# Optimization experiments

Hardware: AMD Instinct MI355X
Metric: run time of the kernel (lower is better)

The kernel has to match this reference:

```python
import jax, jax.numpy as jnp
import numpy as np

N = 100000
E = 1600000
IN_CH = 128
HID = 16
HEADS = 4
OUT_CH = 2
EDGE_DIM = 3
NEG_SLOPE = 0.2


def gat_layer(x, src, dst, e_feat, W, att_src, att_dst, We, att_edge, bias, H, C, concat):
    # x: [N, Fin] -> projected [N, H, C]
    xs = (x @ W).reshape(-1, H, C)
    a_src = jnp.sum(xs * att_src, axis=-1)          # [N, H]
    a_dst = jnp.sum(xs * att_dst, axis=-1)          # [N, H]
    ee = (e_feat @ We).reshape(-1, H, C)            # [E, H, C]
    a_edge = jnp.sum(ee * att_edge, axis=-1)        # [E, H]
    alpha = a_src[src] + a_dst[dst] + a_edge        # [E, H]
    alpha = jax.nn.leaky_relu(alpha, NEG_SLOPE)
    # segment softmax over incoming edges of each dst node
    seg_max = jax.ops.segment_max(alpha, dst, num_segments=N)
    alpha = jnp.exp(alpha - seg_max[dst])
    seg_sum = jax.ops.segment_sum(alpha, dst, num_segments=N)
    alpha = alpha / (seg_sum[dst] + 1e-16)
    # weighted message aggregation
    msg = xs[src] * alpha[:, :, None]               # [E, H, C]
    out = jax.ops.segment_sum(msg, dst, num_segments=N)  # [N, H, C]
    out = out.reshape(-1, H * C) if concat else out.mean(axis=1)
    return out + bias


def setup_inputs() -> dict:
    key = jax.random.key(0)
    ks = jax.random.split(key, 24)
    g = lambda i, shape, scale=0.1: jax.random.normal(ks[i], shape, dtype=jnp.float32) * scale
    inp = {
        "x": jax.random.normal(ks[0], (N, IN_CH), dtype=jnp.float32),
        "edge_index": jax.random.randint(ks[1], (2, E), 0, N, dtype=jnp.int32),
        "edge_feat": jax.random.normal(ks[2], (E, EDGE_DIM), dtype=jnp.float32),
        # edge MLP
        "Em1": g(3, (EDGE_DIM, EDGE_DIM)), "eb1": g(4, (EDGE_DIM,)),
        "Em2": g(5, (EDGE_DIM, EDGE_DIM)), "eb2": g(6, (EDGE_DIM,)),
        # conv1: in -> HID per head, HEADS heads, concat
        "W1": g(7, (IN_CH, HEADS * HID)),
        "as1": g(8, (HEADS, HID)), "ad1": g(9, (HEADS, HID)),
        "We1": g(10, (EDGE_DIM, HEADS * HID)), "ae1": g(11, (HEADS, HID)),
        "b1": g(12, (HEADS * HID,)),
        # conv2: HEADS*HID -> OUT_CH, 1 head, no concat
        "W2": g(13, (HEADS * HID, OUT_CH)),
        "as2": g(14, (1, OUT_CH)), "ad2": g(15, (1, OUT_CH)),
        "We2": g(16, (EDGE_DIM, OUT_CH)), "ae2": g(17, (1, OUT_CH)),
        "b2": g(18, (OUT_CH,)),
    }
    return inp


def reference(x, edge_index, edge_feat,
              Em1, eb1, Em2, eb2,
              W1, as1, ad1, We1, ae1, b1,
              W2, as2, ad2, We2, ae2, b2):
    src, dst = edge_index[0], edge_index[1]
    # edge MLP: Linear -> ReLU -> Linear
    e = jax.nn.relu(edge_feat @ Em1 + eb1) @ Em2 + eb2
    # dropout layers are identity in eval mode
    h = gat_layer(x, src, dst, e, W1, as1, ad1, We1, ae1, b1, HEADS, HID, concat=True)
    h = jax.nn.elu(h)
    out = gat_layer(h, src, dst, e, W2, as2, ad2, We2, ae2, b2, 1, OUT_CH, concat=False)
    return out
```

## Files before the change

### kernel.cpp

```cpp
#include <hip/hip_runtime.h>
#include <hip/hip_fp16.h>
#include <math.h>
#include <stdint.h>

#define NEG_SLOPE 0.2f
#define SCAN_TILE 2048

__device__ __forceinline__ float leaky(float a) { return a > 0.f ? a : NEG_SLOPE * a; }
__device__ __forceinline__ __half2 u2h2(unsigned u) { return *reinterpret_cast<__half2*>(&u); }

__global__ __launch_bounds__(256) void k_pw(const int* __restrict__ dst, int* __restrict__ deg8,
                                            int* __restrict__ pw, int E, int N,
                                            const float* __restrict__ We1, const float* __restrict__ ae1,
                                            const float* __restrict__ We2, const float* __restrict__ ae2,
                                            float* __restrict__ cw) {
    if (blockIdx.x == 0 && threadIdx.x == 0) {
        for (int i = 0; i < 3; i++)
            for (int h = 0; h < 4; h++) {
                float s = 0.f;
                for (int m = 0; m < 16; m++) s += We1[i*64 + h*16 + m] * ae1[h*16 + m];
                cw[i*4 + h] = s;
            }
        for (int i = 0; i < 3; i++) cw[12 + i] = We2[i*2]*ae2[0] + We2[i*2+1]*ae2[1];
    }
    int c = blockIdx.x & 7;
    int* deg = deg8 + (size_t)c * N;
    unsigned ctag = (unsigned)c << 28;
    int base = (blockIdx.x * blockDim.x + threadIdx.x) * 4;
    if (base >= E) return;
    if (base + 3 < E) {
        int4 dv = *reinterpret_cast<const int4*>(&dst[base]);
        int4 pv;
        pv.x = atomicAdd(&deg[dv.x], 1) | ctag;
        pv.y = atomicAdd(&deg[dv.y], 1) | ctag;
        pv.z = atomicAdd(&deg[dv.z], 1) | ctag;
        pv.w = atomicAdd(&deg[dv.w], 1) | ctag;
        *reinterpret_cast<int4*>(&pw[base]) = pv;
    } else {
        for (int i = base; i < E; i++) pw[i] = atomicAdd(&deg[dst[i]], 1) | ctag;
    }
}

__global__ __launch_bounds__(256) void k_scan_partial(const int* __restrict__ deg8, int* __restrict__ tsum, int N) {
    __shared__ int sh[256];
    int b = blockIdx.x, t = threadIdx.x;
    int base = b * SCAN_TILE + t * 8;
    int s = 0;
    if (base + 8 <= N) {
        for (int c = 0; c < 8; c++) {
            const int4* p4 = reinterpret_cast<const int4*>(deg8 + (size_t)c * N + base);
            int4 a = p4[0], bb = p4[1];
            s += a.x + a.y + a.z + a.w + bb.x + bb.y + bb.z + bb.w;
        }
    } else if (base < N) {
        for (int i = base; i < N; i++)
            for (int c = 0; c < 8; c++) s += deg8[(size_t)c * N + i];
    }
    sh[t] = s; __syncthreads();
    for (int o = 128; o > 0; o >>= 1) { if (t < o) sh[t] += sh[t + o]; __syncthreads(); }
    if (t == 0) tsum[b] = sh[0];
}

__global__ void k_scan_tsum(const int* __restrict__ tsum, int* __restrict__ toff,
                            int* __restrict__ rowptr, int nb, int N) {
    if (threadIdx.x == 0 && blockIdx.x == 0) {
        int run = 0;
        for (int i = 0; i < nb; i++) { toff[i] = run; run += tsum[i]; }
        rowptr[N] = run;
    }
}

__global__ __launch_bounds__(256) void k_scan_final(const int* __restrict__ deg8, const int* __restrict__ toff,
        int* __restrict__ rowptr, uint4* __restrict__ slotrec, int N) {
    __shared__ int sh[256];
    int b = blockIdx.x, t = threadIdx.x;
    int base = b * SCAN_TILE + t * 8;
    int vt[8]; int s = 0;
    #pragma unroll
    for (int i = 0; i < 8; i++) {
        int idx = base + i; int tot = 0;
        if (idx < N) {
            #pragma unroll
            for (int c = 0; c < 8; c++) tot += deg8[(size_t)c * N + idx];
        }
        vt[i] = tot; s += tot;
    }
    sh[t] = s; __syncthreads();
    for (int o = 1; o < 256; o <<= 1) {
        int u = (t >= o) ? sh[t - o] : 0;
        __syncthreads();
        sh[t] += u;
        __syncthreads();
    }
    int run = sh[t] - s + toff[b];
    #pragma unroll
    for (int i = 0; i < 8; i++) {
        int idx = base + i;
        if (idx < N) {
            rowptr[idx] = run;
            unsigned lo = 0, hi = 0; int off = 0;
            #pragma unroll
            for (int c = 0; c < 8; c++) {
                unsigned v = (unsigned)off & 0xFFu;
                if (c < 4) lo |= v << (8*c); else hi |= v << (8*(c-4));
                off += deg8[(size_t)c * N + idx];
            }
            slotrec[idx] = make_uint4((unsigned)run, lo, hi, 0u);
            run += vt[i];
        }
    }
}

__global__ __launch_bounds__(256) void k_proj1(const float* __restrict__ x, const float* __restrict__ W1,
        const float* __restrict__ as1, const float* __restrict__ ad1,
        __half* __restrict__ xs1h, float* __restrict__ as1v, float* __restrict__ ad1v, int N) {
    __shared__ float xr[32][128];
    int tid = threadIdx.x;
    int wave = tid >> 6, lane = tid & 63;
    int nbase = blockIdx.x * 32;
    if (nbase + 32 <= N) {
        const float4* x4 = reinterpret_cast<const float4*>(x + (size_t)nbase * 128);
        #pragma unroll
        for (int i = 0; i < 4; i++) {
            int idx = tid + i * 256;
            reinterpret_cast<float4*>(&xr[0][0])[idx] = x4[idx];
        }
    } else {
        for (int i = 0; i < 16; i++) {
            int flat = tid + i * 256;
            int row = flat >> 7, col = flat & 127;
            int n = nbase + row; if (n >= N) n = N - 1;
            xr[row][col] = x[(size_t)n * 128 + col];
        }
    }
    __syncthreads();
    int cc = lane & 15, kk = lane >> 4;
    int nw = wave * 8;
    const float4* W4 = reinterpret_cast<const float4*>(W1);
    float4 acc[8];
    #pragma unroll
    for (int m = 0; m < 8; m++) acc[m] = make_float4(0.f, 0.f, 0.f, 0.f);
    #pragma unroll 4
    for (int k = kk; k < 128; k += 4) {
        float4 wv = W4[k * 16 + cc];
        #pragma unroll
        for (int m = 0; m < 8; m++) {
            float xv = xr[nw + m][k];
            acc[m].x = fmaf(xv, wv.x, acc[m].x);
            acc[m].y = fmaf(xv, wv.y, acc[m].y);
            acc[m].z = fmaf(xv, wv.z, acc[m].z);
            acc[m].w = fmaf(xv, wv.w, acc[m].w);
        }
    }
    float a_s0 = as1[4*cc], a_s1 = as1[4*cc+1], a_s2 = as1[4*cc+2], a_s3 = as1[4*cc+3];
    float a_d0 = ad1[4*cc], a_d1 = ad1[4*cc+1], a_d2 = ad1[4*cc+2], a_d3 = ad1[4*cc+3];
    #pragma unroll
    for (int m = 0; m < 8; m++) {
        float4 a = acc[m];
        a.x += __shfl_xor(a.x, 16, 64); a.y += __shfl_xor(a.y, 16, 64);
        a.z += __shfl_xor(a.z, 16, 64); a.w += __shfl_xor(a.w, 16, 64);
        a.x += __shfl_xor(a.x, 32, 64); a.y += __shfl_xor(a.y, 32, 64);
        a.z += __shfl_xor(a.z, 32, 64); a.w += __shfl_xor(a.w, 32, 64);
        float ps = a.x*a_s0 + a.y*a_s1 + a.z*a_s2 + a.w*a_s3;
        float pd = a.x*a_d0 + a.y*a_d1 + a.z*a_d2 + a.w*a_d3;
        ps += __shfl_xor(ps, 1, 64); ps += __shfl_xor(ps, 2, 64);
        pd += __shfl_xor(pd, 1, 64); pd += __shfl_xor(pd, 2, 64);
        if (kk == 0) {
            int n = nbase + nw + m; if (n >= N) n = N - 1;
            __half2 h01 = __halves2half2(__float2half_rn(a.x), __float2half_rn(a.y));
            __half2 h23 = __halves2half2(__float2half_rn(a.z), __float2half_rn(a.w));
            uint2 st;
            st.x = *reinterpret_cast<unsigned*>(&h01);
            st.y = *reinterpret_cast<unsigned*>(&h23);
            *reinterpret_cast<uint2*>(&xs1h[(size_t)n*64 + 4*cc]) = st;
            if ((cc & 3) == 0) {
                int h = cc >> 2;
                as1v[n*4 + h] = ps;
                ad1v[n*4 + h] = pd;
            }
        }
    }
}

__global__ __launch_bounds__(256) void k_payload(const float* __restrict__ ef,
                       const float* __restrict__ Em1, const float* __restrict__ eb1,
                       const float* __restrict__ Em2, const float* __restrict__ eb2,
                       const float* __restrict__ cw,
                       const int* __restrict__ src, const int* __restrict__ dst,
                       const int* __restrict__ pw,
                       const float4* __restrict__ as1v4,
                       const uint4* __restrict__ slotrec,
                       uint4* __restrict__ csr_pk, int E) {
    int base = (blockIdx.x * blockDim.x + threadIdx.x) * 4;
    if (base >= E) return;
    int cnt = min(4, E - base);

    float f[4][3]; int sv[4], dv[4], pv[4];
    if (cnt == 4) {
        const float4* ef4 = reinterpret_cast<const float4*>(ef);
        float4 a = ef4[base*3/4 + 0], b = ef4[base*3/4 + 1], c = ef4[base*3/4 + 2];
        f[0][0]=a.x; f[0][1]=a.y; f[0][2]=a.z;
        f[1][0]=a.w; f[1][1]=b.x; f[1][2]=b.y;
        f[2][0]=b.z; f[2][1]=b.w; f[2][2]=c.x;
        f[3][0]=c.y; f[3][1]=c.z; f[3][2]=c.w;
        int4 s4 = *reinterpret_cast<const int4*>(&src[base]);
        int4 d4 = *reinterpret_cast<const int4*>(&dst[base]);
        int4 p4 = *reinterpret_cast<const int4*>(&pw[base]);
        sv[0]=s4.x; sv[1]=s4.y; sv[2]=s4.z; sv[3]=s4.w;
        dv[0]=d4.x; dv[1]=d4.y; dv[2]=d4.z; dv[3]=d4.w;
        pv[0]=p4.x; pv[1]=p4.y; pv[2]=p4.z; pv[3]=p4.w;
    } else {
        for (int i = 0; i < cnt; i++) {
            f[i][0]=ef[(base+i)*3+0]; f[i][1]=ef[(base+i)*3+1]; f[i][2]=ef[(base+i)*3+2];
            sv[i]=src[base+i]; dv[i]=dst[base+i]; pv[i]=pw[base+i];
        }
    }

    #pragma unroll
    for (int i = 0; i < 4; i++) {
        if (i >= cnt) break;
        float f0=f[i][0], f1=f[i][1], f2=f[i][2];
        float t0 = fmaxf(f0*Em1[0]+f1*Em1[3]+f2*Em1[6]+eb1[0], 0.f);
        float t1 = fmaxf(f0*Em1[1]+f1*Em1[4]+f2*Em1[7]+eb1[1], 0.f);
        float t2 = fmaxf(f0*Em1[2]+f1*Em1[5]+f2*Em1[8]+eb1[2], 0.f);
        float u0 = t0*Em2[0]+t1*Em2[3]+t2*Em2[6]+eb2[0];
        float u1 = t0*Em2[1]+t1*Em2[4]+t2*Em2[7]+eb2[1];
        float u2 = t0*Em2[2]+t1*Em2[5]+t2*Em2[8]+eb2[2];
        int s = sv[i], d = dv[i];
        float4 av = as1v4[s];
        uint4  r  = slotrec[d];
        int c  = ((unsigned)pv[i]) >> 28;
        int ps = pv[i] & 0x0FFFFFFF;
        unsigned pre = ((c < 4) ? (r.y >> (8*c)) : (r.z >> (8*(c-4)))) & 0xFFu;
        int slot = (int)r.x + (int)pre + ps;
        float b0 = av.x + u0*cw[0] + u1*cw[4] + u2*cw[8];
        float b1 = av.y + u0*cw[1] + u1*cw[5] + u2*cw[9];
        float b2 = av.z + u0*cw[2] + u1*cw[6] + u2*cw[10];
        float b3 = av.w + u0*cw[3] + u1*cw[7] + u2*cw[11];
        float e2 = u0*cw[12] + u1*cw[13] + u2*cw[14];
        __half2 lo = __halves2half2(__float2half_rn(b0), __float2half_rn(b1));
        __half2 hi = __halves2half2(__float2half_rn(b2), __float2half_rn(b3));
        uint4 pki;
        pki.x = (unsigned)s;
        pki.y = *reinterpret_cast<unsigned*>(&lo);
        pki.z = *reinterpret_cast<unsigned*>(&hi);
        pki.w = *reinterpret_cast<unsigned*>(&e2);
        csr_pk[slot] = pki;
    }
}

__global__ __launch_bounds__(256, 4) void k_gat1(
        const int* __restrict__ rowptr, const uint4* __restrict__ csr_pk,
        const __half* __restrict__ xs1h, const float4* __restrict__ ad1v4,
        const float* __restrict__ b1, const float* __restrict__ W2,
        const float* __restrict__ as2, const float* __restrict__ ad2,
        float2* __restrict__ pk2, float* __restrict__ ad2v, int N) {
    int wave = threadIdx.x >> 6, lane = threadIdx.x & 63;
    int d = blockIdx.x * 4 + wave;
    if (d >= N) return;
    int beg = rowptr[d], end = rowptr[d+1];
    float4 ad4 = ad1v4[d];
    int sub = lane & 15;
    int hh  = lane >> 4;
    int e4  = (lane >> 2) & 3;
    int cq  = lane & 3;
    float adh = (hh == 0) ? ad4.x : (hh == 1) ? ad4.y : (hh == 2) ? ad4.z : ad4.w;
    const __half* xbase = xs1h + (hh * 16 + cq * 4);
    float4 acc = make_float4(0.f, 0.f, 0.f, 0.f);
    float wsum = 0.f;
    for (int off = beg; off < end; off += 16) {
        int j = off + sub;
        bool valid = j < end;
        uint4 p = valid ? csr_pk[j] : make_uint4(0u, 0u, 0u, 0u);
        int si = (int)p.x;
        float w = 0.f;
        if (valid) {
            unsigned lw = (hh < 2) ? p.y : p.z;
            __half2 lh = u2h2(lw);
            float lg = (hh & 1) ? __high2float(lh) : __low2float(lh);
            w = __expf(leaky(lg + adh));
        }
        wsum += w;
        int st0 = __shfl(si, e4 + 0, 16);
        int st1 = __shfl(si, e4 + 4, 16);
        int st2 = __shfl(si, e4 + 8, 16);
        int st3 = __shfl(si, e4 + 12, 16);
        float wt0 = __shfl(w, e4 + 0, 16);
        float wt1 = __shfl(w, e4 + 4, 16);
        float wt2 = __shfl(w, e4 + 8, 16);
        float wt3 = __shfl(w, e4 + 12, 16);
        uint2 g0 = *reinterpret_cast<const uint2*>(xbase + ((size_t)st0 << 6));
        uint2 g1 = *reinterpret_cast<const uint2*>(xbase + ((size_t)st1 << 6));
        uint2 g2 = *reinterpret_cast<const uint2*>(xbase + ((size_t)st2 << 6));
        uint2 g3 = *reinterpret_cast<const uint2*>(xbase + ((size_t)st3 << 6));
        __half2 a, b;
        a = u2h2(g0.x); b = u2h2(g0.y);
        acc.x = fmaf(wt0, __low2float(a), acc.x); acc.y = fmaf(wt0, __high2float(a), acc.y);
        acc.z = fmaf(wt0, __low2float(b), acc.z); acc.w = fmaf(wt0, __high2float(b), acc.w);
        a = u2h2(g1.x); b = u2h2(g1.y);
        acc.x = fmaf(wt1, __low2float(a), acc.x); acc.y = fmaf(wt1, __high2float(a), acc.y);
        acc.z = fmaf(wt1, __low2float(b), acc.z); acc.w = fmaf(wt1, __high2float(b), acc.w);
        a = u2h2(g2.x); b = u2h2(g2.y);
        acc.x = fmaf(wt2, __low2float(a), acc.x); acc.y = fmaf(wt2, __high2float(a), acc.y);
        acc.z = fmaf(wt2, __low2float(b), acc.z); acc.w = fmaf(wt2, __high2float(b), acc.w);
        a = u2h2(g3.x); b = u2h2(g3.y);
        acc.x = fmaf(wt3, __low2float(a), acc.x); acc.y = fmaf(wt3, __high2float(a), acc.y);
        acc.z = fmaf(wt3, __low2float(b), acc.z); acc.w = fmaf(wt3, __high2float(b), acc.w);
    }
    acc.x += __shfl_xor(acc.x, 4, 64); acc.y += __shfl_xor(acc.y, 4, 64);
    acc.z += __shfl_xor(acc.z, 4, 64); acc.w += __shfl_xor(acc.w, 4, 64);
    acc.x += __shfl_xor(acc.x, 8, 64); acc.y += __shfl_xor(acc.y, 8, 64);
    acc.z += __shfl_xor(acc.z, 8, 64); acc.w += __shfl_xor(acc.w, 8, 64);
    wsum += __shfl_xor(wsum, 1, 64);
    wsum += __shfl_xor(wsum, 2, 64);
    wsum += __shfl_xor(wsum, 4, 64);
    wsum += __shfl_xor(wsum, 8, 64);
    float inv = 1.f / (wsum + 1e-16f);
    float p0 = 0.f, p1 = 0.f;
    if (e4 == 0) {
        int cb = hh * 16 + cq * 4;
        float v0 = acc.x * inv + b1[cb + 0];
        float v1 = acc.y * inv + b1[cb + 1];
        float v2 = acc.z * inv + b1[cb + 2];
        float v3 = acc.w * inv + b1[cb + 3];
        v0 = v0 > 0.f ? v0 : expm1f(v0);
        v1 = v1 > 0.f ? v1 : expm1f(v1);
        v2 = v2 > 0.f ? v2 : expm1f(v2);
        v3 = v3 > 0.f ? v3 : expm1f(v3);
        p0 = v0*W2[(cb+0)*2]   + v1*W2[(cb+1)*2]   + v2*W2[(cb+2)*2]   + v3*W2[(cb+3)*2];
        p1 = v0*W2[(cb+0)*2+1] + v1*W2[(cb+1)*2+1] + v2*W2[(cb+2)*2+1] + v3*W2[(cb+3)*2+1];
    }
    p0 += __shfl_xor(p0, 1, 64);  p1 += __shfl_xor(p1, 1, 64);
    p0 += __shfl_xor(p0, 2, 64);  p1 += __shfl_xor(p1, 2, 64);
    p0 += __shfl_xor(p0, 16, 64); p1 += __shfl_xor(p1, 16, 64);
    p0 += __shfl_xor(p0, 32, 64); p1 += __shfl_xor(p1, 32, 64);
    if (lane == 0) {
        float2 q;
        q.x = p0*as2[0] + p1*as2[1];
        __half2 xv = __halves2half2(__float2half_rn(p0), __float2half_rn(p1));
        q.y = *reinterpret_cast<float*>(&xv);
        pk2[d] = q;
        ad2v[d] = p0*ad2[0] + p1*ad2[1];
    }
}

__global__ __launch_bounds__(256) void k_gat2(
        const int* __restrict__ rowptr, const uint4* __restrict__ csr_pk,
        const float2* __restrict__ pk2, const float* __restrict__ ad2v,
        const float* __restrict__ b2, float* __restrict__ out, int N) {
    int t = blockIdx.x * blockDim.x + threadIdx.x;
    int d = t >> 4, j16 = t & 15;
    if (d >= N) return;
    int beg = rowptr[d], end = rowptr[d+1];
    float add = ad2v[d];
    float sm = 0.f, p0 = 0.f, p1 = 0.f;
    for (int off = beg; off < end; off += 16) {
        int j = off + j16;
        if (j < end) {
            uint4 p = csr_pk[j];
            int s = (int)p.x;
            float ea2 = *reinterpret_cast<float*>(&p.w);
            float2 q = pk2[s];
            float w = __expf(leaky(q.x + add + ea2));
            __half2 xv = *reinterpret_cast<__half2*>(&q.y);
            p0 = fmaf(w, __low2float(xv), p0);
            p1 = fmaf(w, __high2float(xv), p1);
            sm += w;
        }
    }
    #pragma unroll
    for (int o = 1; o < 16; o <<= 1) {
        sm += __shfl_xor(sm, o, 16);
        p0 += __shfl_xor(p0, o, 16);
        p1 += __shfl_xor(p1, o, 16);
    }
    if (j16 == 0) {
        float inv = 1.f / (sm + 1e-16f);
        out[d*2+0] = p0*inv + b2[0];
        out[d*2+1] = p1*inv + b2[1];
    }
}

extern "C" void kernel_launch(void* const* d_in, const int* in_sizes, int n_in,
                              void* d_out, int out_size, void* d_ws, size_t ws_size,
                              hipStream_t stream) {
    const float* x   = (const float*)d_in[0];
    const int*   ei  = (const int*)d_in[1];
    const float* ef  = (const float*)d_in[2];
    const float* Em1 = (const float*)d_in[3];
    const float* eb1 = (const float*)d_in[4];
    const float* Em2 = (const float*)d_in[5];
    const float* eb2 = (const float*)d_in[6];
    const float* W1  = (const float*)d_in[7];
    const float* as1 = (const float*)d_in[8];
    const float* ad1 = (const float*)d_in[9];
    const float* We1 = (const float*)d_in[10];
    const float* ae1 = (const float*)d_in[11];
    const float* b1  = (const float*)d_in[12];
    const float* W2  = (const float*)d_in[13];
    const float* as2 = (const float*)d_in[14];
    const float* ad2 = (const float*)d_in[15];
    const float* We2 = (const float*)d_in[16];
    const float* ae2 = (const float*)d_in[17];
    const float* b2  = (const float*)d_in[18];

    const int N = in_sizes[0] / 128;
    const int E = in_sizes[1] / 2;
    const int* srcp = ei;
    const int* dstp = ei + E;

    uintptr_t w = (uintptr_t)d_ws;
    auto alloc = [&](size_t bytes) -> void* {
        uintptr_t p = w; w += (bytes + 255) & ~(size_t)255; return (void*)p;
    };
    const int nb = (N + SCAN_TILE - 1) / SCAN_TILE;
    int*    deg8    = (int*)alloc((size_t)8 * N * sizeof(int));
    int*    rowptr  = (int*)alloc(((size_t)N + 1) * sizeof(int));
    int*    tsum    = (int*)alloc((size_t)nb * sizeof(int));
    int*    toff    = (int*)alloc((size_t)(nb + 1) * sizeof(int));
    float*  cw      = (float*)alloc(16 * sizeof(float));
    int*    pw      = (int*)alloc((size_t)E * sizeof(int));
    uint4*  slotrec = (uint4*)alloc((size_t)N * sizeof(uint4));
    uint4*  csr_pk  = (uint4*)alloc((size_t)E * sizeof(uint4));
    __half* xs1h    = (__half*)alloc((size_t)N * 64 * sizeof(__half));
    float*  as1v    = (float*)alloc((size_t)N * 4 * sizeof(float));
    float*  ad1v    = (float*)alloc((size_t)N * 4 * sizeof(float));
    float2* pk2     = (float2*)alloc((size_t)N * sizeof(float2));
    float*  ad2v    = (float*)alloc((size_t)N * sizeof(float));

    const int B = 256;

    hipMemsetAsync(deg8, 0, (size_t)8 * N * sizeof(int), stream);
    k_pw<<<(E/4+B-1)/B + 1, B, 0, stream>>>(dstp, deg8, pw, E, N, We1, ae1, We2, ae2, cw);
    k_scan_partial<<<nb, 256, 0, stream>>>(deg8, tsum, N);
    k_scan_tsum<<<1, 64, 0, stream>>>(tsum, toff, rowptr, nb, N);
    k_scan_final<<<nb, 256, 0, stream>>>(deg8, toff, rowptr, slotrec, N);
    k_proj1<<<(N+31)/32, 256, 0, stream>>>(x, W1, as1, ad1, xs1h, as1v, ad1v, N);
    k_payload<<<(E/4+B-1)/B + 1, B, 0, stream>>>(ef, Em1, eb1, Em2, eb2, cw,
                                                 srcp, dstp, pw, (const float4*)as1v,
                                                 slotrec, csr_pk, E);
    k_gat1<<<(N+3)/4, 256, 0, stream>>>(rowptr, csr_pk, xs1h, (const float4*)ad1v,
                                        b1, W2, as2, ad2, pk2, ad2v, N);
    k_gat2<<<(N*16+B-1)/B, B, 0, stream>>>(rowptr, csr_pk, pk2, ad2v, b2, (float*)d_out, N);
}
```

Baseline: 254.1 us.

## Fuse degree counting into projection kernel and widen payload to 8 edges

Merges the atomic degree-counting kernel into the node projection kernel. Blocks are interleaved by a period so that every `period`-th block does edge atomics (8 edges per thread) and the rest compute the x@W1 projection. The atomic-latency-bound work and the compute/bandwidth-bound projection can then share the GPU at once, and one launch is saved. Separately, the payload kernel now handles 8 edges per thread and issues the as1v and slotrec gathers for 4 edges before using them, to expose more memory-level parallelism. The cost is more register pressure in the payload kernel and idle tail projection blocks.

```diff
diff --git a/kernel.cpp b/kernel.cpp
--- a/kernel.cpp
+++ b/kernel.cpp
@@ -9,115 +9,55 @@
 __device__ __forceinline__ float leaky(float a) { return a > 0.f ? a : NEG_SLOPE * a; }
 __device__ __forceinline__ __half2 u2h2(unsigned u) { return *reinterpret_cast<__half2*>(&u); }
 
-__global__ __launch_bounds__(256) void k_pw(const int* __restrict__ dst, int* __restrict__ deg8,
-                                            int* __restrict__ pw, int E, int N,
-                                            const float* __restrict__ We1, const float* __restrict__ ae1,
-                                            const float* __restrict__ We2, const float* __restrict__ ae2,
-                                            float* __restrict__ cw) {
-    if (blockIdx.x == 0 && threadIdx.x == 0) {
-        for (int i = 0; i < 3; i++)
-            for (int h = 0; h < 4; h++) {
-                float s = 0.f;
-                for (int m = 0; m < 16; m++) s += We1[i*64 + h*16 + m] * ae1[h*16 + m];
-                cw[i*4 + h] = s;
-            }
-        for (int i = 0; i < 3; i++) cw[12 + i] = We2[i*2]*ae2[0] + We2[i*2+1]*ae2[1];
-    }
-    int c = blockIdx.x & 7;
-    int* deg = deg8 + (size_t)c * N;
-    unsigned ctag = (unsigned)c << 28;
-    int base = (blockIdx.x * blockDim.x + threadIdx.x) * 4;
-    if (base >= E) return;
-    if (base + 3 < E) {
-        int4 dv = *reinterpret_cast<const int4*>(&dst[base]);
-        int4 pv;
-        pv.x = atomicAdd(&deg[dv.x], 1) | ctag;
-        pv.y = atomicAdd(&deg[dv.y], 1) | ctag;
-        pv.z = atomicAdd(&deg[dv.z], 1) | ctag;
-        pv.w = atomicAdd(&deg[dv.w], 1) | ctag;
-        *reinterpret_cast<int4*>(&pw[base]) = pv;
-    } else {
-        for (int i = base; i < E; i++) pw[i] = atomicAdd(&deg[dst[i]], 1) | ctag;
-    }
-}
-
-__global__ __launch_bounds__(256) void k_scan_partial(const int* __restrict__ deg8, int* __restrict__ tsum, int N) {
-    __shared__ int sh[256];
-    int b = blockIdx.x, t = threadIdx.x;
-    int base = b * SCAN_TILE + t * 8;
-    int s = 0;
-    if (base + 8 <= N) {
-        for (int c = 0; c < 8; c++) {
-            const int4* p4 = reinterpret_cast<const int4*>(deg8 + (size_t)c * N + base);
-            int4 a = p4[0], bb = p4[1];
-            s += a.x + a.y + a.z + a.w + bb.x + bb.y + bb.z + bb.w;
-        }
-    } else if (base < N) {
-        for (int i = base; i < N; i++)
-            for (int c = 0; c < 8; c++) s += deg8[(size_t)c * N + i];
-    }
-    sh[t] = s; __syncthreads();
-    for (int o = 128; o > 0; o >>= 1) { if (t < o) sh[t] += sh[t + o]; __syncthreads(); }
-    if (t == 0) tsum[b] = sh[0];
-}
-
-__global__ void k_scan_tsum(const int* __restrict__ tsum, int* __restrict__ toff,
-                            int* __restrict__ rowptr, int nb, int N) {
-    if (threadIdx.x == 0 && blockIdx.x == 0) {
-        int run = 0;
-        for (int i = 0; i < nb; i++) { toff[i] = run; run += tsum[i]; }
-        rowptr[N] = run;
-    }
-}
-
-__global__ __launch_bounds__(256) void k_scan_final(const int* __restrict__ deg8, const int* __restrict__ toff,
-        int* __restrict__ rowptr, uint4* __restrict__ slotrec, int N) {
-    __shared__ int sh[256];
-    int b = blockIdx.x, t = threadIdx.x;
-    int base = b * SCAN_TILE + t * 8;
-    int vt[8]; int s = 0;
-    #pragma unroll
-    for (int i = 0; i < 8; i++) {
-        int idx = base + i; int tot = 0;
-        if (idx < N) {
-            #pragma unroll
-            for (int c = 0; c < 8; c++) tot += deg8[(size_t)c * N + idx];
-        }
-        vt[i] = tot; s += tot;
-    }
-    sh[t] = s; __syncthreads();
-    for (int o = 1; o < 256; o <<= 1) {
-        int u = (t >= o) ? sh[t - o] : 0;
-        __syncthreads();
-        sh[t] += u;
-        __syncthreads();
-    }
-    int run = sh[t] - s + toff[b];
-    #pragma unroll
-    for (int i = 0; i < 8; i++) {
-        int idx = base + i;
-        if (idx < N) {
-            rowptr[idx] = run;
-            unsigned lo = 0, hi = 0; int off = 0;
-            #pragma unroll
-            for (int c = 0; c < 8; c++) {
-                unsigned v = (unsigned)off & 0xFFu;
-                if (c < 4) lo |= v << (8*c); else hi |= v << (8*(c-4));
-                off += deg8[(size_t)c * N + idx];
-            }
-            slotrec[idx] = make_uint4((unsigned)run, lo, hi, 0u);
-            run += vt[i];
-        }
-    }
-}
-
-__global__ __launch_bounds__(256) void k_proj1(const float* __restrict__ x, const float* __restrict__ W1,
+__global__ __launch_bounds__(256) void k_pwproj(
+        const float* __restrict__ x, const float* __restrict__ W1,
         const float* __restrict__ as1, const float* __restrict__ ad1,
-        __half* __restrict__ xs1h, float* __restrict__ as1v, float* __restrict__ ad1v, int N) {
+        __half* __restrict__ xs1h, float* __restrict__ as1v, float* __restrict__ ad1v, int N,
+        const int* __restrict__ dst, int* __restrict__ deg8, int* __restrict__ pw, int E,
+        const float* __restrict__ We1, const float* __restrict__ ae1,
+        const float* __restrict__ We2, const float* __restrict__ ae2,
+        float* __restrict__ cw, int period) {
     __shared__ float xr[32][128];
+    int bx = blockIdx.x;
+    if (bx % period == period - 1) {
+        int pb = bx / period;
+        if (pb == 0 && threadIdx.x == 0) {
+            for (int i = 0; i < 3; i++)
+                for (int h = 0; h < 4; h++) {
+                    float s = 0.f;
+                    for (int m = 0; m < 16; m++) s += We1[i*64 + h*16 + m] * ae1[h*16 + m];
+                    cw[i*4 + h] = s;
+                }
+            for (int i = 0; i < 3; i++) cw[12 + i] = We2[i*2]*ae2[0] + We2[i*2+1]*ae2[1];
+        }
+        int c = pb & 7;
+        int* deg = deg8 + (size_t)c * N;
+        unsigned ctag = (unsigned)c << 28;
+        int base = (pb * 256 + (int)threadIdx.x) * 8;
+        if (base >= E) return;
+        if (base + 7 < E) {
+            int4 d0 = *reinterpret_cast<const int4*>(&dst[base]);
+            int4 d1 = *reinterpret_cast<const int4*>(&dst[base + 4]);
+            int4 p0, p1;
+            p0.x = atomicAdd(&deg[d0.x], 1) | ctag;
+            p0.y = atomicAdd(&deg[d0.y], 1) | ctag;
+            p0.z = atomicAdd(&deg[d0.z], 1) | ctag;
+            p0.w = atomicAdd(&deg[d0.w], 1) | ctag;
+            p1.x = atomicAdd(&deg[d1.x], 1) | ctag;
+            p1.y = atomicAdd(&deg[d1.y], 1) | ctag;
+            p1.z = atomicAdd(&deg[d1.z], 1) | ctag;
+            p1.w = atomicAdd(&deg[d1.w], 1) | ctag;
+            *reinterpret_cast<int4*>(&pw[base]) = p0;
+            *reinterpret_cast<int4*>(&pw[base + 4]) = p1;
+        } else {
+            for (int i = base; i < E; i++) pw[i] = atomicAdd(&deg[dst[i]], 1) | ctag;
+        }
+        return;
+    }
+    int pb = bx - bx / period;
     int tid = threadIdx.x;
     int wave = tid >> 6, lane = tid & 63;
-    int nbase = blockIdx.x * 32;
+    int nbase = pb * 32;
     if (nbase + 32 <= N) {
         const float4* x4 = reinterpret_cast<const float4*>(x + (size_t)nbase * 128);
         #pragma unroll
@@ -182,6 +122,76 @@
     }
 }
 
+__global__ __launch_bounds__(256) void k_scan_partial(const int* __restrict__ deg8, int* __restrict__ tsum, int N) {
+    __shared__ int sh[256];
+    int b = blockIdx.x, t = threadIdx.x;
+    int base = b * SCAN_TILE + t * 8;
+    int s = 0;
+    if (base + 8 <= N) {
+        for (int c = 0; c < 8; c++) {
+            const int4* p4 = reinterpret_cast<const int4*>(deg8 + (size_t)c * N + base);
+            int4 a = p4[0], bb = p4[1];
+            s += a.x + a.y + a.z + a.w + bb.x + bb.y + bb.z + bb.w;
+        }
+    } else if (base < N) {
+        for (int i = base; i < N; i++)
+            for (int c = 0; c < 8; c++) s += deg8[(size_t)c * N + i];
+    }
+    sh[t] = s; __syncthreads();
+    for (int o = 128; o > 0; o >>= 1) { if (t < o) sh[t] += sh[t + o]; __syncthreads(); }
+    if (t == 0) tsum[b] = sh[0];
+}
+
+__global__ void k_scan_tsum(const int* __restrict__ tsum, int* __restrict__ toff,
+                            int* __restrict__ rowptr, int nb, int N) {
+    if (threadIdx.x == 0 && blockIdx.x == 0) {
+        int run = 0;
+        for (int i = 0; i < nb; i++) { toff[i] = run; run += tsum[i]; }
+        rowptr[N] = run;
+    }
+}
+
+__global__ __launch_bounds__(256) void k_scan_final(const int* __restrict__ deg8, const int* __restrict__ toff,
+        int* __restrict__ rowptr, uint4* __restrict__ slotrec, int N) {
+    __shared__ int sh[256];
+    int b = blockIdx.x, t = threadIdx.x;
+    int base = b * SCAN_TILE + t * 8;
+    int vt[8]; int s = 0;
+    #pragma unroll
+    for (int i = 0; i < 8; i++) {
+        int idx = base + i; int tot = 0;
+        if (idx < N) {
+            #pragma unroll
+            for (int c = 0; c < 8; c++) tot += deg8[(size_t)c * N + idx];
+        }
+        vt[i] = tot; s += tot;
+    }
+    sh[t] = s; __syncthreads();
+    for (int o = 1; o < 256; o <<= 1) {
+        int u = (t >= o) ? sh[t - o] : 0;
+        __syncthreads();
+        sh[t] += u;
+        __syncthreads();
+    }
+    int run = sh[t] - s + toff[b];
+    #pragma unroll
+    for (int i = 0; i < 8; i++) {
+        int idx = base + i;
+        if (idx < N) {
+            rowptr[idx] = run;
+            unsigned lo = 0, hi = 0; int off = 0;
+            #pragma unroll
+            for (int c = 0; c < 8; c++) {
+                unsigned v = (unsigned)off & 0xFFu;
+                if (c < 4) lo |= v << (8*c); else hi |= v << (8*(c-4));
+                off += deg8[(size_t)c * N + idx];
+            }
+            slotrec[idx] = make_uint4((unsigned)run, lo, hi, 0u);
+            run += vt[i];
+        }
+    }
+}
+
 __global__ __launch_bounds__(256) void k_payload(const float* __restrict__ ef,
                        const float* __restrict__ Em1, const float* __restrict__ eb1,
                        const float* __restrict__ Em2, const float* __restrict__ eb2,
@@ -191,61 +201,79 @@
                        const float4* __restrict__ as1v4,
                        const uint4* __restrict__ slotrec,
                        uint4* __restrict__ csr_pk, int E) {
-    int base = (blockIdx.x * blockDim.x + threadIdx.x) * 4;
+    int base = (blockIdx.x * blockDim.x + threadIdx.x) * 8;
     if (base >= E) return;
-    int cnt = min(4, E - base);
-
-    float f[4][3]; int sv[4], dv[4], pv[4];
-    if (cnt == 4) {
+    int cnt = min(8, E - base);
+
+    float fl[24]; int sv[8], dv[8], pv[8];
+    if (cnt == 8) {
         const float4* ef4 = reinterpret_cast<const float4*>(ef);
-        float4 a = ef4[base*3/4 + 0], b = ef4[base*3/4 + 1], c = ef4[base*3/4 + 2];
-        f[0][0]=a.x; f[0][1]=a.y; f[0][2]=a.z;
-        f[1][0]=a.w; f[1][1]=b.x; f[1][2]=b.y;
-        f[2][0]=b.z; f[2][1]=b.w; f[2][2]=c.x;
-        f[3][0]=c.y; f[3][1]=c.z; f[3][2]=c.w;
-        int4 s4 = *reinterpret_cast<const int4*>(&src[base]);
-        int4 d4 = *reinterpret_cast<const int4*>(&dst[base]);
-        int4 p4 = *reinterpret_cast<const int4*>(&pw[base]);
-        sv[0]=s4.x; sv[1]=s4.y; sv[2]=s4.z; sv[3]=s4.w;
-        dv[0]=d4.x; dv[1]=d4.y; dv[2]=d4.z; dv[3]=d4.w;
-        pv[0]=p4.x; pv[1]=p4.y; pv[2]=p4.z; pv[3]=p4.w;
+        int b6 = (base >> 2) * 3;
+        #pragma unroll
+        for (int i = 0; i < 6; i++) {
+            float4 q = ef4[b6 + i];
+            fl[i*4+0] = q.x; fl[i*4+1] = q.y; fl[i*4+2] = q.z; fl[i*4+3] = q.w;
+        }
+        int4 s0 = *reinterpret_cast<const int4*>(&src[base]);
+        int4 s1 = *reinterpret_cast<const int4*>(&src[base+4]);
+        int4 d0 = *reinterpret_cast<const int4*>(&dst[base]);
+        int4 d1 = *reinterpret_cast<const int4*>(&dst[base+4]);
+        int4 q0 = *reinterpret_cast<const int4*>(&pw[base]);
+        int4 q1 = *reinterpret_cast<const int4*>(&pw[base+4]);
+        sv[0]=s0.x; sv[1]=s0.y; sv[2]=s0.z; sv[3]=s0.w; sv[4]=s1.x; sv[5]=s1.y; sv[6]=s1.z; sv[7]=s1.w;
+        dv[0]=d0.x; dv[1]=d0.y; dv[2]=d0.z; dv[3]=d0.w; dv[4]=d1.x; dv[5]=d1.y; dv[6]=d1.z; dv[7]=d1.w;
+        pv[0]=q0.x; pv[1]=q0.y; pv[2]=q0.z; pv[3]=q0.w; pv[4]=q1.x; pv[5]=q1.y; pv[6]=q1.z; pv[7]=q1.w;
     } else {
         for (int i = 0; i < cnt; i++) {
-            f[i][0]=ef[(base+i)*3+0]; f[i][1]=ef[(base+i)*3+1]; f[i][2]=ef[(base+i)*3+2];
+            fl[i*3+0]=ef[(base+i)*3+0]; fl[i*3+1]=ef[(base+i)*3+1]; fl[i*3+2]=ef[(base+i)*3+2];
             sv[i]=src[base+i]; dv[i]=dst[base+i]; pv[i]=pw[base+i];
         }
     }
 
     #pragma unroll
-    for (int i = 0; i < 4; i++) {
-        if (i >= cnt) break;
-        float f0=f[i][0], f1=f[i][1], f2=f[i][2];
-        float t0 = fmaxf(f0*Em1[0]+f1*Em1[3]+f2*Em1[6]+eb1[0], 0.f);
-        float t1 = fmaxf(f0*Em1[1]+f1*Em1[4]+f2*Em1[7]+eb1[1], 0.f);
-        float t2 = fmaxf(f0*Em1[2]+f1*Em1[5]+f2*Em1[8]+eb1[2], 0.f);
-        float u0 = t0*Em2[0]+t1*Em2[3]+t2*Em2[6]+eb2[0];
-        float u1 = t0*Em2[1]+t1*Em2[4]+t2*Em2[7]+eb2[1];
-        float u2 = t0*Em2[2]+t1*Em2[5]+t2*Em2[8]+eb2[2];
-        int s = sv[i], d = dv[i];
-        float4 av = as1v4[s];
-        uint4  r  = slotrec[d];
-        int c  = ((unsigned)pv[i]) >> 28;
-        int ps = pv[i] & 0x0FFFFFFF;
-        unsigned pre = ((c < 4) ? (r.y >> (8*c)) : (r.z >> (8*(c-4)))) & 0xFFu;
-        int slot = (int)r.x + (int)pre + ps;
-        float b0 = av.x + u0*cw[0] + u1*cw[4] + u2*cw[8];
-        float b1 = av.y + u0*cw[1] + u1*cw[5] + u2*cw[9];
-        float b2 = av.z + u0*cw[2] + u1*cw[6] + u2*cw[10];
-        float b3 = av.w + u0*cw[3] + u1*cw[7] + u2*cw[11];
-        float e2 = u0*cw[12] + u1*cw[13] + u2*cw[14];
-        __half2 lo = __halves2half2(__float2half_rn(b0), __float2half_rn(b1));
-        __half2 hi = __halves2half2(__float2half_rn(b2), __float2half_rn(b3));
-        uint4 pki;
-        pki.x = (unsigned)s;
-        pki.y = *reinterpret_cast<unsigned*>(&lo);
-        pki.z = *reinterpret_cast<unsigned*>(&hi);
-        pki.w = *reinterpret_cast<unsigned*>(&e2);
-        csr_pk[slot] = pki;
+    for (int half = 0; half < 2; half++) {
+        int i0 = half * 4;
+        if (i0 >= cnt) break;
+        float4 av[4]; uint4 rr[4];
+        #pragma unroll
+        for (int k = 0; k < 4; k++) {
+            int i = i0 + k;
+            int s = (i < cnt) ? sv[i] : sv[0];
+            int d = (i < cnt) ? dv[i] : dv[0];
+            av[k] = as1v4[s];
+            rr[k] = slotrec[d];
+        }
+        #pragma unroll
+        for (int k = 0; k < 4; k++) {
+            int i = i0 + k;
+            if (i >= cnt) break;
+            float f0 = fl[i*3+0], f1 = fl[i*3+1], f2 = fl[i*3+2];
+            float t0 = fmaxf(f0*Em1[0]+f1*Em1[3]+f2*Em1[6]+eb1[0], 0.f);
+            float t1 = fmaxf(f0*Em1[1]+f1*Em1[4]+f2*Em1[7]+eb1[1], 0.f);
+            float t2 = fmaxf(f0*Em1[2]+f1*Em1[5]+f2*Em1[8]+eb1[2], 0.f);
+            float u0 = t0*Em2[0]+t1*Em2[3]+t2*Em2[6]+eb2[0];
+            float u1 = t0*Em2[1]+t1*Em2[4]+t2*Em2[7]+eb2[1];
+            float u2 = t0*Em2[2]+t1*Em2[5]+t2*Em2[8]+eb2[2];
+            float4 avk = av[k];
+            uint4  r   = rr[k];
+            int c  = ((unsigned)pv[i]) >> 28;
+            int ps = pv[i] & 0x0FFFFFFF;
+            unsigned pre = ((c < 4) ? (r.y >> (8*c)) : (r.z >> (8*(c-4)))) & 0xFFu;
+            int slot = (int)r.x + (int)pre + ps;
+            float b0 = avk.x + u0*cw[0] + u1*cw[4] + u2*cw[8];
+            float b1 = avk.y + u0*cw[1] + u1*cw[5] + u2*cw[9];
+            float b2 = avk.z + u0*cw[2] + u1*cw[6] + u2*cw[10];
+            float b3 = avk.w + u0*cw[3] + u1*cw[7] + u2*cw[11];
+            float e2 = u0*cw[12] + u1*cw[13] + u2*cw[14];
+            __half2 lo = __halves2half2(__float2half_rn(b0), __float2half_rn(b1));
+            __half2 hi = __halves2half2(__float2half_rn(b2), __float2half_rn(b3));
+            uint4 pki;
+            pki.x = (unsigned)sv[i];
+            pki.y = *reinterpret_cast<unsigned*>(&lo);
+            pki.z = *reinterpret_cast<unsigned*>(&hi);
+            pki.w = *reinterpret_cast<unsigned*>(&e2);
+            csr_pk[slot] = pki;
+        }
     }
 }
 
@@ -431,12 +459,16 @@
     const int B = 256;
 
     hipMemsetAsync(deg8, 0, (size_t)8 * N * sizeof(int), stream);
-    k_pw<<<(E/4+B-1)/B + 1, B, 0, stream>>>(dstp, deg8, pw, E, N, We1, ae1, We2, ae2, cw);
+    int npwb   = ((E + 7) / 8 + B - 1) / B;
+    int nprojb = (N + 31) / 32;
+    int period = (nprojb + npwb - 1) / npwb + 1;
+    int grid_f = npwb * period;
+    k_pwproj<<<grid_f, B, 0, stream>>>(x, W1, as1, ad1, xs1h, as1v, ad1v, N,
+                                       dstp, deg8, pw, E, We1, ae1, We2, ae2, cw, period);
     k_scan_partial<<<nb, 256, 0, stream>>>(deg8, tsum, N);
     k_scan_tsum<<<1, 64, 0, stream>>>(tsum, toff, rowptr, nb, N);
     k_scan_final<<<nb, 256, 0, stream>>>(deg8, toff, rowptr, slotrec, N);
-    k_proj1<<<(N+31)/32, 256, 0, stream>>>(x, W1, as1, ad1, xs1h, as1v, ad1v, N);
-    k_payload<<<(E/4+B-1)/B + 1, B, 0, stream>>>(ef, Em1, eb1, Em2, eb2, cw,
+    k_payload<<<(E/8+B-1)/B + 1, B, 0, stream>>>(ef, Em1, eb1, Em2, eb2, cw,
                                                  srcp, dstp, pw, (const float4*)as1v,
                                                  slotrec, csr_pk, E);
     k_gat1<<<(N+3)/4, 256, 0, stream>>>(rowptr, csr_pk, xs1h, (const float4*)ad1v,
```

Result: faster. 245.2 us (-3.5%).
